# Performance work log

Hardware: AMD Instinct MI355X
Metric: run time of the kernel (lower is better)

The kernel has to match this reference:

```python
import jax, jax.numpy as jnp
import numpy as np

V, H = 30522, 768
B, S = 64, 512
NEW_ROWS = 10004          # 1 pad + num_labels(10000) + depth(2) + 1
N_NODES = NEW_ROWS - 2    # rows [1:-1] of new_embedding go through the graph
N_SOFT = 8
N_EDGES = 50000
LEAKY_SLOPE = 0.2


def setup_inputs() -> dict:
    key = jax.random.key(0)
    ks = jax.random.split(key, 8)
    x = jax.random.randint(ks[0], (B, S), 0, V + NEW_ROWS - 1, dtype=jnp.int64)
    edge_index = jax.random.randint(ks[1], (2, N_EDGES), 0, N_NODES, dtype=jnp.int64)
    original_weight = jax.random.normal(ks[2], (V, H), jnp.float32) * 0.02
    new_weight = jax.random.normal(ks[3], (NEW_ROWS, H), jnp.float32) * 0.02
    new_weight = new_weight.at[0].set(0.0)  # padding row prepended in __init__
    soft_prompt_weight = jax.random.normal(ks[4], (N_SOFT, H), jnp.float32) * 0.02
    W_gat = jax.random.normal(ks[5], (H, H), jnp.float32) / np.sqrt(H)
    a_src = jax.random.normal(ks[6], (H,), jnp.float32) * 0.05
    a_dst = jax.random.normal(ks[7], (H,), jnp.float32) * 0.05
    return {"x": x, "edge_index": edge_index, "original_weight": original_weight,
            "new_weight": new_weight, "soft_prompt_weight": soft_prompt_weight,
            "W_gat": W_gat, "a_src": a_src, "a_dst": a_dst}


def _gat_layer(feat, W_gat, a_src, a_dst, edge_index):
    """Single-head GAT over label graph: gather-attend-scatter. feat: [N, H]."""
    n = feat.shape[0]
    h = feat @ W_gat                                   # [N, H]
    src, dst = edge_index[0], edge_index[1]            # [E], [E]
    s_src = h @ a_src                                  # [N]
    s_dst = h @ a_dst                                  # [N]
    e = jax.nn.leaky_relu(s_src[src] + s_dst[dst], LEAKY_SLOPE)   # [E]
    # segment softmax over incoming edges of each dst node
    m = jax.ops.segment_max(e, dst, num_segments=n)
    ex = jnp.exp(e - m[dst])
    denom = jax.ops.segment_sum(ex, dst, num_segments=n)
    alpha = ex / (denom[dst] + 1e-16)                  # [E]
    agg = jax.ops.segment_sum(alpha[:, None] * h[src], dst, num_segments=n)  # [N, H]
    return feat + agg                                  # residual connection


def _combined_weight(original_weight, new_weight, W_gat, a_src, a_dst, edge_index):
    edge_features = new_weight[1:-1]                   # [N_NODES, H]
    edge_features = _gat_layer(edge_features, W_gat, a_src, a_dst, edge_index)
    edge_features = jnp.concatenate([edge_features, new_weight[-1:]], axis=0)
    return jnp.concatenate([original_weight, edge_features], axis=0)  # [V+NEW_ROWS-1, H]


def reference(x, edge_index, original_weight, new_weight, soft_prompt_weight,
              W_gat, a_src, a_dst):
    bsz = x.shape[0]
    weight = _combined_weight(original_weight, new_weight, W_gat, a_src, a_dst, edge_index)
    other_emb = weight[x[:, N_SOFT:]]                  # [B, S-N_SOFT, H] big gather
    soft = jnp.broadcast_to(soft_prompt_weight[None], (bsz, N_SOFT, H))
    return jnp.concatenate([soft, other_emb], axis=1)  # [B, S, H]
```

## Files before the change

kernel.cpp:

```cpp
#include <hip/hip_runtime.h>
#include <stdint.h>

#define HDIM  768
#define VOCAB 30522
#define NNODE 10002
#define NEDGE 50000
#define NROWS 10004
#define SLOPE 0.2f

constexpr size_t SZ_HB     = (size_t)NNODE * HDIM * 2;
constexpr size_t SZ_F32    = (size_t)NNODE * HDIM * 4;
constexpr size_t OFF_H     = 0;
constexpr size_t OFF_FB    = OFF_H  + SZ_HB;
constexpr size_t OFF_FO    = OFF_FB + SZ_HB;
constexpr size_t OFF_WT    = OFF_FO + SZ_F32;
constexpr size_t SZ_WT     = (size_t)HDIM * HDIM * 2;
constexpr size_t OFF_WAS   = OFF_WT + SZ_WT;
constexpr size_t OFF_WAD   = OFF_WAS + HDIM * 4;
constexpr size_t OFF_SS    = OFF_WAD + HDIM * 4;
constexpr size_t SZ_N4     = 40032;
constexpr size_t OFF_SD    = OFF_SS  + SZ_N4;
constexpr size_t OFF_CNT   = OFF_SD  + SZ_N4;
constexpr size_t OFF_START = OFF_CNT + SZ_N4;
constexpr size_t OFF_CUR   = OFF_START + SZ_N4;
constexpr size_t OFF_ESRC  = OFF_CUR + SZ_N4;
constexpr size_t OFF_ESC   = OFF_ESRC + NEDGE * 4;

__device__ __forceinline__ unsigned short f2bf(float f) {
  unsigned int u = __float_as_uint(f);
  u += 0x7FFFu + ((u >> 16) & 1u);
  return (unsigned short)(u >> 16);
}
__device__ __forceinline__ float bf2f(unsigned short b) {
  return __uint_as_float(((unsigned int)b) << 16);
}

typedef __attribute__((ext_vector_type(8))) short bf16x8;
typedef __attribute__((ext_vector_type(4))) float f32x4;

__device__ __forceinline__ void gl2lds16(const unsigned short* g, unsigned short* l) {
  __builtin_amdgcn_global_load_lds(
      (const __attribute__((address_space(1))) unsigned int*)g,
      (__attribute__((address_space(3))) unsigned int*)l, 16, 0, 0);
}

__global__ __launch_bounds__(256) void k_prep(const float* __restrict__ W,
                                              const float* __restrict__ a_s,
                                              const float* __restrict__ a_d,
                                              unsigned short* __restrict__ wT,
                                              float* __restrict__ wa_s,
                                              float* __restrict__ wa_d) {
  int bid = blockIdx.x, tid = threadIdx.x;
  if (bid < 576) {
    __shared__ float tile[32][33];
    int tx0 = (bid % 24) * 32, ty0 = (bid / 24) * 32;
    int cx = tid & 31, cy = tid >> 5;
#pragma unroll
    for (int r = 0; r < 4; ++r)
      tile[cy + r * 8][cx] = W[(size_t)(ty0 + cy + r * 8) * HDIM + tx0 + cx];
    __syncthreads();
#pragma unroll
    for (int r = 0; r < 4; ++r)
      wT[(size_t)(tx0 + cy + r * 8) * HDIM + ty0 + cx] = f2bf(tile[cx][cy + r * 8]);
  } else {
    int lane = tid & 63, wid = tid >> 6;
    int row = (bid - 576) * 4 + wid;
    float ss = 0.f, sd = 0.f;
    for (int n = lane; n < HDIM; n += 64) {
      float w = W[(size_t)row * HDIM + n];
      ss += w * a_s[n];
      sd += w * a_d[n];
    }
#pragma unroll
    for (int off = 32; off; off >>= 1) {
      ss += __shfl_down(ss, off, 64);
      sd += __shfl_down(sd, off, 64);
    }
    if (lane == 0) { wa_s[row] = ss; wa_d[row] = sd; }
  }
}

__global__ __launch_bounds__(256) void k_convert_scores(const float* __restrict__ feat,
                                                        const float* __restrict__ wa_s,
                                                        const float* __restrict__ wa_d,
                                                        unsigned short* __restrict__ featbf,
                                                        float* __restrict__ s_s,
                                                        float* __restrict__ s_d) {
  int lane = threadIdx.x & 63, wid = threadIdx.x >> 6;
  int r = blockIdx.x * 4 + wid;
  if (r >= NNODE) return;
  const float4* fr = (const float4*)(feat + (size_t)r * HDIM);
  ushort4* ob = (ushort4*)(featbf + (size_t)r * HDIM);
  float ss = 0.f, sd = 0.f;
#pragma unroll
  for (int i = 0; i < 3; ++i) {
    int c = lane + i * 64;
    float4 v = fr[c];
    float4 vs = ((const float4*)wa_s)[c];
    float4 vd = ((const float4*)wa_d)[c];
    ss += v.x * vs.x + v.y * vs.y + v.z * vs.z + v.w * vs.w;
    sd += v.x * vd.x + v.y * vd.y + v.z * vd.z + v.w * vd.w;
    ushort4 o;
    o.x = f2bf(v.x); o.y = f2bf(v.y); o.z = f2bf(v.z); o.w = f2bf(v.w);
    ob[c] = o;
  }
#pragma unroll
  for (int off = 32; off; off >>= 1) {
    ss += __shfl_down(ss, off, 64);
    sd += __shfl_down(sd, off, 64);
  }
  if (lane == 0) { s_s[r] = ss; s_d[r] = sd; }
}

__global__ __launch_bounds__(256) void k_gemm(const unsigned short* __restrict__ A,
                                              const unsigned short* __restrict__ BT,
                                              unsigned short* __restrict__ Hout) {
  __shared__ __align__(16) unsigned short As[128 * 32];
  __shared__ __align__(16) unsigned short Bs[128 * 32];
  int tid = threadIdx.x, lane = tid & 63, wid = tid >> 6;
  int m0 = blockIdx.x * 128, n0 = blockIdx.y * 128;
  int wm = wid >> 1, wn = wid & 1;
  int q = lane >> 4, lr = lane & 15;

  f32x4 acc[4][4];
#pragma unroll
  for (int i = 0; i < 4; ++i)
#pragma unroll
    for (int j = 0; j < 4; ++j) acc[i][j] = 0.f;

  for (int kt = 0; kt < 24; ++kt) {
    int k0 = kt * 32;
#pragma unroll
    for (int t = 0; t < 2; ++t) {
      int c = wid * 128 + t * 64 + lane;
      int row = c >> 2, kk = (c & 3) << 3;
      int grow = m0 + row;
      grow = grow <= NNODE - 1 ? grow : NNODE - 1;
      gl2lds16(A + (size_t)grow * HDIM + k0 + kk, As + (size_t)wid * 1024 + t * 512);
      int nrow = n0 + row;
      gl2lds16(BT + (size_t)nrow * HDIM + k0 + kk, Bs + (size_t)wid * 1024 + t * 512);
    }
    __syncthreads();
    bf16x8 a[4], b[4];
#pragma unroll
    for (int i = 0; i < 4; ++i)
      a[i] = *(const bf16x8*)(As + (wm * 64 + i * 16 + lr) * 32 + q * 8);
#pragma unroll
    for (int j = 0; j < 4; ++j)
      b[j] = *(const bf16x8*)(Bs + (wn * 64 + j * 16 + lr) * 32 + q * 8);
#pragma unroll
    for (int i = 0; i < 4; ++i)
#pragma unroll
      for (int j = 0; j < 4; ++j)
        acc[i][j] = __builtin_amdgcn_mfma_f32_16x16x32_bf16(a[i], b[j], acc[i][j], 0, 0, 0);
    __syncthreads();
  }
#pragma unroll
  for (int i = 0; i < 4; ++i) {
    int mbase = m0 + wm * 64 + i * 16 + q * 4;
#pragma unroll
    for (int j = 0; j < 4; ++j) {
      int n = n0 + wn * 64 + j * 16 + lr;
#pragma unroll
      for (int rg = 0; rg < 4; ++rg) {
        int m = mbase + rg;
        if (m < NNODE) Hout[(size_t)m * HDIM + n] = f2bf(acc[i][j][rg]);
      }
    }
  }
}

__global__ __launch_bounds__(256) void k_hist(const int* __restrict__ ei,
                                              int* __restrict__ count) {
  int e = blockIdx.x * 256 + threadIdx.x;
  if (e >= NEDGE) return;
  atomicAdd(count + ei[NEDGE + e], 1);
}

__global__ __launch_bounds__(256) void k_scan(const int* __restrict__ count,
                                              int* __restrict__ start,
                                              int* __restrict__ cursor) {
  __shared__ int part[256];
  int tid = threadIdx.x;
  int base = tid * 40;
  int loc[40];
  int s = 0;
#pragma unroll
  for (int i = 0; i < 40; ++i) {
    int idx = base + i;
    int c = (idx < NNODE) ? count[idx] : 0;
    loc[i] = s; s += c;
  }
  part[tid] = s;
  __syncthreads();
  for (int d = 1; d < 256; d <<= 1) {
    int t = (tid >= d) ? part[tid - d] : 0;
    __syncthreads();
    part[tid] += t;
    __syncthreads();
  }
  int excl = part[tid] - s;
#pragma unroll
  for (int i = 0; i < 40; ++i) {
    int idx = base + i;
    if (idx < NNODE) {
      int v = excl + loc[i];
      start[idx] = v;
      cursor[idx] = v;
    }
  }
  if (tid == 255) start[NNODE] = part[255];
}

__global__ __launch_bounds__(256) void k_scatter(const int* __restrict__ ei,
                                                 const float* __restrict__ s_s,
                                                 const float* __restrict__ s_d,
                                                 int* __restrict__ cursor,
                                                 int* __restrict__ esrc,
                                                 float* __restrict__ escore) {
  int e = blockIdx.x * 256 + threadIdx.x;
  if (e >= NEDGE) return;
  int src = ei[e], dst = ei[NEDGE + e];
  float v = s_s[src] + s_d[dst];
  v = v > 0.f ? v : SLOPE * v;
  int pos = atomicAdd(cursor + dst, 1);
  esrc[pos] = src;
  escore[pos] = v;
}

__global__ __launch_bounds__(256) void k_aggregate(const int* __restrict__ start,
                                                   const int* __restrict__ esrc,
                                                   const float* __restrict__ escore,
                                                   const unsigned short* __restrict__ h,
                                                   const float* __restrict__ feat,
                                                   float* __restrict__ fo) {
  int n = blockIdx.x, t = threadIdx.x;
  int b = start[n], en = start[n + 1];
  float m = -3.4e38f;
  for (int e = b; e < en; ++e) m = fmaxf(m, escore[e]);
  float a0 = 0.f, a1 = 0.f, a2 = 0.f, den = 0.f;
  for (int e = b; e < en; ++e) {
    float ex = __expf(escore[e] - m);
    den += ex;
    const unsigned short* hr = h + (size_t)esrc[e] * HDIM;
    a0 += ex * bf2f(hr[t]);
    a1 += ex * bf2f(hr[t + 256]);
    a2 += ex * bf2f(hr[t + 512]);
  }
  float inv = 1.f / (den + 1e-16f);
  size_t o = (size_t)n * HDIM + t;
  fo[o]       = feat[o]       + a0 * inv;
  fo[o + 256] = feat[o + 256] + a1 * inv;
  fo[o + 512] = feat[o + 512] + a2 * inv;
}

__global__ __launch_bounds__(256) void k_gather(const int* __restrict__ x,
                                                const float* __restrict__ orig,
                                                const float* __restrict__ nw,
                                                const float* __restrict__ soft,
                                                const float* __restrict__ fo,
                                                uint4* __restrict__ out) {
  int chunk = blockIdx.x * 256 + threadIdx.x;
  int row = chunk / 192;
  int c4 = chunk - row * 192;
  int s = row & 511;
  const float* g;
  if (s < 8) {
    g = soft + (size_t)s * HDIM + c4 * 4;
  } else {
    int idx = x[row];
    if (idx < VOCAB) g = orig + (size_t)idx * HDIM + c4 * 4;
    else if (idx < VOCAB + NNODE) g = fo + (size_t)(idx - VOCAB) * HDIM + c4 * 4;
    else g = nw + (size_t)(NROWS - 1) * HDIM + c4 * 4;
  }
  out[chunk] = *(const uint4*)g;
}

extern "C" void kernel_launch(void* const* d_in, const int* in_sizes, int n_in,
                              void* d_out, int out_size, void* d_ws, size_t ws_size,
                              hipStream_t stream) {
  const int* x    = (const int*)d_in[0];
  const int* ei   = (const int*)d_in[1];
  const float* og = (const float*)d_in[2];
  const float* nw = (const float*)d_in[3];
  const float* sp = (const float*)d_in[4];
  const float* W  = (const float*)d_in[5];
  const float* as = (const float*)d_in[6];
  const float* ad = (const float*)d_in[7];
  const float* feat = nw + HDIM;

  char* ws = (char*)d_ws;
  unsigned short* hbuf   = (unsigned short*)(ws + OFF_H);
  unsigned short* featbf = (unsigned short*)(ws + OFF_FB);
  float* fo              = (float*)(ws + OFF_FO);
  unsigned short* wT     = (unsigned short*)(ws + OFF_WT);
  float* wa_s            = (float*)(ws + OFF_WAS);
  float* wa_d            = (float*)(ws + OFF_WAD);
  float* s_s             = (float*)(ws + OFF_SS);
  float* s_d             = (float*)(ws + OFF_SD);
  int* count             = (int*)(ws + OFF_CNT);
  int* startArr          = (int*)(ws + OFF_START);
  int* cursor            = (int*)(ws + OFF_CUR);
  int* esrc              = (int*)(ws + OFF_ESRC);
  float* escore          = (float*)(ws + OFF_ESC);

  (void)hipMemsetAsync(count, 0, SZ_N4, stream);
  k_prep<<<768, 256, 0, stream>>>(W, as, ad, wT, wa_s, wa_d);
  k_convert_scores<<<(NNODE + 3) / 4, 256, 0, stream>>>(feat, wa_s, wa_d, featbf, s_s, s_d);
  k_gemm<<<dim3(79, 6), 256, 0, stream>>>(featbf, wT, hbuf);
  k_hist<<<(NEDGE + 255) / 256, 256, 0, stream>>>(ei, count);
  k_scan<<<1, 256, 0, stream>>>(count, startArr, cursor);
  k_scatter<<<(NEDGE + 255) / 256, 256, 0, stream>>>(ei, s_s, s_d, cursor, esrc, escore);
  k_aggregate<<<NNODE, 256, 0, stream>>>(startArr, esrc, escore, hbuf, feat, fo);
  k_gather<<<(32768 * 192) / 256, 256, 0, stream>>>(x, og, nw, sp, fo, (uint4*)d_out);
}
```

Measured before the change: 298.0 us.

## Fuse graph preprocessing kernels into GEMM and prep launches, retile GEMM, vectorize aggregate

Merges the edge histogram into the weight-prep kernel, the CSR scan into the convert/score kernel, and the edge scatter into the GEMM kernel as extra blocks, cutting the launch count from eight to five. The GEMM tile shrinks from 128x128 to 128x64 so more blocks cover the device. The aggregate kernel now uses 192 threads, each loading four bf16 values and one float4 at a time. The dependencies still hold because each merged piece runs one launch after its inputs, and the tail kernels are unchanged.

```diff
diff --git a/kernel.cpp b/kernel.cpp
--- a/kernel.cpp
+++ b/kernel.cpp
@@ -44,13 +44,20 @@
       (__attribute__((address_space(3))) unsigned int*)l, 16, 0, 0);
 }
 
-__global__ __launch_bounds__(256) void k_prep(const float* __restrict__ W,
-                                              const float* __restrict__ a_s,
-                                              const float* __restrict__ a_d,
-                                              unsigned short* __restrict__ wT,
-                                              float* __restrict__ wa_s,
-                                              float* __restrict__ wa_d) {
+__global__ __launch_bounds__(256) void k_front(const float* __restrict__ W,
+                                               const float* __restrict__ a_s,
+                                               const float* __restrict__ a_d,
+                                               const int* __restrict__ ei,
+                                               unsigned short* __restrict__ wT,
+                                               float* __restrict__ wa_s,
+                                               float* __restrict__ wa_d,
+                                               int* __restrict__ count) {
   int bid = blockIdx.x, tid = threadIdx.x;
+  if (bid >= 768) {
+    int e = (bid - 768) * 256 + tid;
+    if (e < NEDGE) atomicAdd(count + ei[NEDGE + e], 1);
+    return;
+  }
   if (bid < 576) {
     __shared__ float tile[32][33];
     int tx0 = (bid % 24) * 32, ty0 = (bid / 24) * 32;
@@ -80,12 +87,48 @@
   }
 }
 
-__global__ __launch_bounds__(256) void k_convert_scores(const float* __restrict__ feat,
-                                                        const float* __restrict__ wa_s,
-                                                        const float* __restrict__ wa_d,
-                                                        unsigned short* __restrict__ featbf,
-                                                        float* __restrict__ s_s,
-                                                        float* __restrict__ s_d) {
+__global__ __launch_bounds__(256) void k_mid(const float* __restrict__ feat,
+                                             const float* __restrict__ wa_s,
+                                             const float* __restrict__ wa_d,
+                                             unsigned short* __restrict__ featbf,
+                                             float* __restrict__ s_s,
+                                             float* __restrict__ s_d,
+                                             const int* __restrict__ count,
+                                             int* __restrict__ startArr,
+                                             int* __restrict__ cursor) {
+  if (blockIdx.x == 2501) {
+    __shared__ int part[256];
+    int tid = threadIdx.x;
+    int base = tid * 40;
+    int loc[40];
+    int s = 0;
+#pragma unroll
+    for (int i = 0; i < 40; ++i) {
+      int idx = base + i;
+      int c = (idx < NNODE) ? count[idx] : 0;
+      loc[i] = s; s += c;
+    }
+    part[tid] = s;
+    __syncthreads();
+    for (int d = 1; d < 256; d <<= 1) {
+      int t = (tid >= d) ? part[tid - d] : 0;
+      __syncthreads();
+      part[tid] += t;
+      __syncthreads();
+    }
+    int excl = part[tid] - s;
+#pragma unroll
+    for (int i = 0; i < 40; ++i) {
+      int idx = base + i;
+      if (idx < NNODE) {
+        int v = excl + loc[i];
+        startArr[idx] = v;
+        cursor[idx] = v;
+      }
+    }
+    if (tid == 255) startArr[NNODE] = part[255];
+    return;
+  }
   int lane = threadIdx.x & 63, wid = threadIdx.x >> 6;
   int r = blockIdx.x * 4 + wid;
   if (r >= NNODE) return;
@@ -112,21 +155,40 @@
   if (lane == 0) { s_s[r] = ss; s_d[r] = sd; }
 }
 
-__global__ __launch_bounds__(256) void k_gemm(const unsigned short* __restrict__ A,
+__global__ __launch_bounds__(256) void k_main(const unsigned short* __restrict__ A,
                                               const unsigned short* __restrict__ BT,
-                                              unsigned short* __restrict__ Hout) {
+                                              unsigned short* __restrict__ Hout,
+                                              const int* __restrict__ ei,
+                                              const float* __restrict__ s_s,
+                                              const float* __restrict__ s_d,
+                                              int* __restrict__ cursor,
+                                              int* __restrict__ esrc,
+                                              float* __restrict__ escore) {
+  int b = blockIdx.x;
+  if (b >= 948) {
+    int e = (b - 948) * 256 + threadIdx.x;
+    if (e < NEDGE) {
+      int src = ei[e], dst = ei[NEDGE + e];
+      float v = s_s[src] + s_d[dst];
+      v = v > 0.f ? v : SLOPE * v;
+      int pos = atomicAdd(cursor + dst, 1);
+      esrc[pos] = src;
+      escore[pos] = v;
+    }
+    return;
+  }
   __shared__ __align__(16) unsigned short As[128 * 32];
-  __shared__ __align__(16) unsigned short Bs[128 * 32];
+  __shared__ __align__(16) unsigned short Bs[64 * 32];
   int tid = threadIdx.x, lane = tid & 63, wid = tid >> 6;
-  int m0 = blockIdx.x * 128, n0 = blockIdx.y * 128;
+  int m0 = (b % 79) * 128, n0 = (b / 79) * 64;
   int wm = wid >> 1, wn = wid & 1;
   int q = lane >> 4, lr = lane & 15;
 
-  f32x4 acc[4][4];
+  f32x4 acc[4][2];
 #pragma unroll
   for (int i = 0; i < 4; ++i)
 #pragma unroll
-    for (int j = 0; j < 4; ++j) acc[i][j] = 0.f;
+    for (int j = 0; j < 2; ++j) acc[i][j] = 0.f;
 
   for (int kt = 0; kt < 24; ++kt) {
     int k0 = kt * 32;
@@ -137,30 +199,33 @@
       int grow = m0 + row;
       grow = grow <= NNODE - 1 ? grow : NNODE - 1;
       gl2lds16(A + (size_t)grow * HDIM + k0 + kk, As + (size_t)wid * 1024 + t * 512);
-      int nrow = n0 + row;
-      gl2lds16(BT + (size_t)nrow * HDIM + k0 + kk, Bs + (size_t)wid * 1024 + t * 512);
+    }
+    {
+      int c = wid * 64 + lane;
+      int row = c >> 2, kk = (c & 3) << 3;
+      gl2lds16(BT + (size_t)(n0 + row) * HDIM + k0 + kk, Bs + (size_t)wid * 512);
     }
     __syncthreads();
-    bf16x8 a[4], b[4];
+    bf16x8 a[4], bb[2];
 #pragma unroll
     for (int i = 0; i < 4; ++i)
       a[i] = *(const bf16x8*)(As + (wm * 64 + i * 16 + lr) * 32 + q * 8);
 #pragma unroll
-    for (int j = 0; j < 4; ++j)
-      b[j] = *(const bf16x8*)(Bs + (wn * 64 + j * 16 + lr) * 32 + q * 8);
+    for (int j = 0; j < 2; ++j)
+      bb[j] = *(const bf16x8*)(Bs + (wn * 32 + j * 16 + lr) * 32 + q * 8);
 #pragma unroll
     for (int i = 0; i < 4; ++i)
 #pragma unroll
-      for (int j = 0; j < 4; ++j)
-        acc[i][j] = __builtin_amdgcn_mfma_f32_16x16x32_bf16(a[i], b[j], acc[i][j], 0, 0, 0);
+      for (int j = 0; j < 2; ++j)
+        acc[i][j] = __builtin_amdgcn_mfma_f32_16x16x32_bf16(a[i], bb[j], acc[i][j], 0, 0, 0);
     __syncthreads();
   }
 #pragma unroll
   for (int i = 0; i < 4; ++i) {
     int mbase = m0 + wm * 64 + i * 16 + q * 4;
 #pragma unroll
-    for (int j = 0; j < 4; ++j) {
-      int n = n0 + wn * 64 + j * 16 + lr;
+    for (int j = 0; j < 2; ++j) {
+      int n = n0 + wn * 32 + j * 16 + lr;
 #pragma unroll
       for (int rg = 0; rg < 4; ++rg) {
         int m = mbase + rg;
@@ -170,65 +235,7 @@
   }
 }
 
-__global__ __launch_bounds__(256) void k_hist(const int* __restrict__ ei,
-                                              int* __restrict__ count) {
-  int e = blockIdx.x * 256 + threadIdx.x;
-  if (e >= NEDGE) return;
-  atomicAdd(count + ei[NEDGE + e], 1);
-}
-
-__global__ __launch_bounds__(256) void k_scan(const int* __restrict__ count,
-                                              int* __restrict__ start,
-                                              int* __restrict__ cursor) {
-  __shared__ int part[256];
-  int tid = threadIdx.x;
-  int base = tid * 40;
-  int loc[40];
-  int s = 0;
-#pragma unroll
-  for (int i = 0; i < 40; ++i) {
-    int idx = base + i;
-    int c = (idx < NNODE) ? count[idx] : 0;
-    loc[i] = s; s += c;
-  }
-  part[tid] = s;
-  __syncthreads();
-  for (int d = 1; d < 256; d <<= 1) {
-    int t = (tid >= d) ? part[tid - d] : 0;
-    __syncthreads();
-    part[tid] += t;
-    __syncthreads();
-  }
-  int excl = part[tid] - s;
-#pragma unroll
-  for (int i = 0; i < 40; ++i) {
-    int idx = base + i;
-    if (idx < NNODE) {
-      int v = excl + loc[i];
-      start[idx] = v;
-      cursor[idx] = v;
-    }
-  }
-  if (tid == 255) start[NNODE] = part[255];
-}
-
-__global__ __launch_bounds__(256) void k_scatter(const int* __restrict__ ei,
-                                                 const float* __restrict__ s_s,
-                                                 const float* __restrict__ s_d,
-                                                 int* __restrict__ cursor,
-                                                 int* __restrict__ esrc,
-                                                 float* __restrict__ escore) {
-  int e = blockIdx.x * 256 + threadIdx.x;
-  if (e >= NEDGE) return;
-  int src = ei[e], dst = ei[NEDGE + e];
-  float v = s_s[src] + s_d[dst];
-  v = v > 0.f ? v : SLOPE * v;
-  int pos = atomicAdd(cursor + dst, 1);
-  esrc[pos] = src;
-  escore[pos] = v;
-}
-
-__global__ __launch_bounds__(256) void k_aggregate(const int* __restrict__ start,
+__global__ __launch_bounds__(192) void k_aggregate(const int* __restrict__ start,
                                                    const int* __restrict__ esrc,
                                                    const float* __restrict__ escore,
                                                    const unsigned short* __restrict__ h,
@@ -238,20 +245,21 @@
   int b = start[n], en = start[n + 1];
   float m = -3.4e38f;
   for (int e = b; e < en; ++e) m = fmaxf(m, escore[e]);
-  float a0 = 0.f, a1 = 0.f, a2 = 0.f, den = 0.f;
+  float a0 = 0.f, a1 = 0.f, a2 = 0.f, a3 = 0.f, den = 0.f;
   for (int e = b; e < en; ++e) {
     float ex = __expf(escore[e] - m);
     den += ex;
-    const unsigned short* hr = h + (size_t)esrc[e] * HDIM;
-    a0 += ex * bf2f(hr[t]);
-    a1 += ex * bf2f(hr[t + 256]);
-    a2 += ex * bf2f(hr[t + 512]);
+    ushort4 hv = *(const ushort4*)(h + (size_t)esrc[e] * HDIM + t * 4);
+    a0 += ex * bf2f(hv.x);
+    a1 += ex * bf2f(hv.y);
+    a2 += ex * bf2f(hv.z);
+    a3 += ex * bf2f(hv.w);
   }
   float inv = 1.f / (den + 1e-16f);
-  size_t o = (size_t)n * HDIM + t;
-  fo[o]       = feat[o]       + a0 * inv;
-  fo[o + 256] = feat[o + 256] + a1 * inv;
-  fo[o + 512] = feat[o + 512] + a2 * inv;
+  size_t o = (size_t)n * HDIM + t * 4;
+  float4 f = *(const float4*)(feat + o);
+  f.x += a0 * inv; f.y += a1 * inv; f.z += a2 * inv; f.w += a3 * inv;
+  *(float4*)(fo + o) = f;
 }
 
 __global__ __launch_bounds__(256) void k_gather(const int* __restrict__ x,
@@ -305,12 +313,11 @@
   float* escore          = (float*)(ws + OFF_ESC);
 
   (void)hipMemsetAsync(count, 0, SZ_N4, stream);
-  k_prep<<<768, 256, 0, stream>>>(W, as, ad, wT, wa_s, wa_d);
-  k_convert_scores<<<(NNODE + 3) / 4, 256, 0, stream>>>(feat, wa_s, wa_d, featbf, s_s, s_d);
-  k_gemm<<<dim3(79, 6), 256, 0, stream>>>(featbf, wT, hbuf);
-  k_hist<<<(NEDGE + 255) / 256, 256, 0, stream>>>(ei, count);
-  k_scan<<<1, 256, 0, stream>>>(count, startArr, cursor);
-  k_scatter<<<(NEDGE + 255) / 256, 256, 0, stream>>>(ei, s_s, s_d, cursor, esrc, escore);
-  k_aggregate<<<NNODE, 256, 0, stream>>>(startArr, esrc, escore, hbuf, feat, fo);
+  k_front<<<964, 256, 0, stream>>>(W, as, ad, ei, wT, wa_s, wa_d, count);
+  k_mid<<<2502, 256, 0, stream>>>(feat, wa_s, wa_d, featbf, s_s, s_d,
+                                  count, startArr, cursor);
+  k_main<<<1144, 256, 0, stream>>>(featbf, wT, hbuf, ei, s_s, s_d,
+                                   cursor, esrc, escore);
+  k_aggregate<<<NNODE, 192, 0, stream>>>(startArr, esrc, escore, hbuf, feat, fo);
   k_gather<<<(32768 * 192) / 256, 256, 0, stream>>>(x, og, nw, sp, fo, (uint4*)d_out);
 }
```

Result: faster. 289.9 us (-2.7%).
